# Performance work log

Measured on AMD Instinct MI355X. Metric: run time of the kernel, lower is better.

## Reference

```python
import jax, jax.numpy as jnp
import numpy as np

DIM = 512
HEADS = 6
DH = 64
INNER = HEADS * DH  # 384
M = 20              # num_landmarks
PINV_ITERS = 6
KERNEL = 33         # residual_conv_kernel
SCALE = DH ** -0.5


def setup_inputs() -> dict:
    key = jax.random.key(0)
    ks = jax.random.split(key, 7)
    x = jax.random.normal(ks[0], (16, 6000, DIM), dtype=jnp.float32)
    norm_w = jnp.ones((DIM,), dtype=jnp.float32)
    norm_b = jnp.zeros((DIM,), dtype=jnp.float32)
    w_qkv = jax.random.normal(ks[1], (DIM, 3 * INNER), dtype=jnp.float32) * 0.02
    w_out = jax.random.normal(ks[2], (INNER, DIM), dtype=jnp.float32) * 0.02
    b_out = jnp.zeros((DIM,), dtype=jnp.float32)
    # depthwise conv over seq dim: torch Conv2d(heads, heads, (33,1), groups=heads)
    res_kernel = jax.random.normal(ks[3], (HEADS, 1, KERNEL, 1), dtype=jnp.float32) * 0.1
    return {"x": x, "norm_w": norm_w, "norm_b": norm_b, "w_qkv": w_qkv,
            "w_out": w_out, "b_out": b_out, "res_kernel": res_kernel}


def moore_penrose_pinv(a, iters=PINV_ITERS):
    # a: [b, h, m, m]
    abs_a = jnp.abs(a)
    denom = abs_a.sum(-1).max() * abs_a.sum(-2).max()  # global maxes, as in torch ref
    z = jnp.swapaxes(a, -1, -2) / denom
    I = jnp.eye(a.shape[-1], dtype=a.dtype)
    for _ in range(iters):
        az = a @ z
        z = 0.25 * z @ (13.0 * I - az @ (15.0 * I - az @ (7.0 * I - az)))
    return z


def nystrom_attention(xn, w_qkv, w_out, b_out, res_kernel):
    b, n, _ = xn.shape
    qkv = xn @ w_qkv  # [b, n, 3*inner]
    q, k, v = jnp.split(qkv, 3, axis=-1)
    to_heads = lambda t: t.reshape(b, n, HEADS, DH).transpose(0, 2, 1, 3)  # b h n d
    q, k, v = to_heads(q), to_heads(k), to_heads(v)
    q = q * SCALE

    l = n // M  # n chosen as multiple of m, so no padding branch
    q_land = q.reshape(b, HEADS, M, l, DH).mean(axis=3)  # b h m d
    k_land = k.reshape(b, HEADS, M, l, DH).mean(axis=3)

    sim1 = jnp.einsum('bhid,bhjd->bhij', q, k_land)       # b h n m
    sim2 = jnp.einsum('bhid,bhjd->bhij', q_land, k_land)  # b h m m
    sim3 = jnp.einsum('bhid,bhjd->bhij', q_land, k)       # b h m n

    attn1 = jax.nn.softmax(sim1, axis=-1)
    attn2 = jax.nn.softmax(sim2, axis=-1)
    attn3 = jax.nn.softmax(sim3, axis=-1)

    attn2_inv = moore_penrose_pinv(attn2)
    out = (attn1 @ attn2_inv) @ (attn3 @ v)  # b h n d

    # residual depthwise conv along seq dim, per head (groups=heads)
    pad = KERNEL // 2
    conv = jax.lax.conv_general_dilated(
        v, res_kernel, window_strides=(1, 1), padding=((pad, pad), (0, 0)),
        dimension_numbers=('NCHW', 'OIHW', 'NCHW'), feature_group_count=HEADS)
    out = out + conv

    out = out.transpose(0, 2, 1, 3).reshape(b, n, INNER)
    return out @ w_out + b_out


def reference(x, norm_w, norm_b, w_qkv, w_out, b_out, res_kernel):
    mu = x.mean(-1, keepdims=True)
    var = jnp.mean((x - mu) ** 2, axis=-1, keepdims=True)
    xn = (x - mu) / jnp.sqrt(var + 1e-5) * norm_w + norm_b
    return x + nystrom_attention(xn, w_qkv, w_out, b_out, res_kernel)
```

## Files before the change

### kernel.cpp

```cpp
#include <hip/hip_runtime.h>

typedef float  f32x4  __attribute__((ext_vector_type(4)));
typedef __bf16 bf16x4 __attribute__((ext_vector_type(4)));
typedef __bf16 bf16x8 __attribute__((ext_vector_type(8)));

#define B_     16
#define N_     6000
#define D_     512
#define H_     6
#define DH_    64
#define INNER_ 384
#define M_     20
#define L_     300
#define KW_    33
#define ROWS_  (B_ * N_)
#define SCALE_ 0.125f
#define CH_    256
#define NCH_   24

__device__ __forceinline__ ushort f2bf(float f) {
    __bf16 h = (__bf16)f;
    return __builtin_bit_cast(ushort, h);
}
__device__ __forceinline__ float bf2f(ushort h) {
    return __uint_as_float(((unsigned)h) << 16);
}

#define GLD(gp, lp) __builtin_amdgcn_global_load_lds( \
    (const __attribute__((address_space(1))) unsigned int*)(gp), \
    (__attribute__((address_space(3))) unsigned int*)(lp), 16, 0, 0)

__global__ __launch_bounds__(256) void ln_kernel(const float* __restrict__ x,
        const float* __restrict__ w, const float* __restrict__ b,
        ushort* __restrict__ xn) {
    int row  = blockIdx.x * 4 + (threadIdx.x >> 6);
    int lane = threadIdx.x & 63;
    const float4* xp = (const float4*)(x + (size_t)row * D_);
    float4 v0 = xp[lane];
    float4 v1 = xp[lane + 64];
    float s  = v0.x + v0.y + v0.z + v0.w + v1.x + v1.y + v1.z + v1.w;
    float sq = v0.x*v0.x + v0.y*v0.y + v0.z*v0.z + v0.w*v0.w
             + v1.x*v1.x + v1.y*v1.y + v1.z*v1.z + v1.w*v1.w;
    #pragma unroll
    for (int o = 32; o; o >>= 1) { s += __shfl_xor(s, o); sq += __shfl_xor(sq, o); }
    float mu   = s * (1.0f / D_);
    float var  = sq * (1.0f / D_) - mu * mu;
    float rstd = rsqrtf(var + 1e-5f);
    const float4 wv0 = ((const float4*)w)[lane];
    const float4 wv1 = ((const float4*)w)[lane + 64];
    const float4 bv0 = ((const float4*)b)[lane];
    const float4 bv1 = ((const float4*)b)[lane + 64];
    ushort4 o0, o1;
    o0.x = f2bf((v0.x - mu) * rstd * wv0.x + bv0.x);
    o0.y = f2bf((v0.y - mu) * rstd * wv0.y + bv0.y);
    o0.z = f2bf((v0.z - mu) * rstd * wv0.z + bv0.z);
    o0.w = f2bf((v0.w - mu) * rstd * wv0.w + bv0.w);
    o1.x = f2bf((v1.x - mu) * rstd * wv1.x + bv1.x);
    o1.y = f2bf((v1.y - mu) * rstd * wv1.y + bv1.y);
    o1.z = f2bf((v1.z - mu) * rstd * wv1.z + bv1.z);
    o1.w = f2bf((v1.w - mu) * rstd * wv1.w + bv1.w);
    ((ushort4*)(xn + (size_t)row * D_))[lane]      = o0;
    ((ushort4*)(xn + (size_t)row * D_))[lane + 64] = o1;
}

__global__ void transpose_cast_kernel(const float* __restrict__ W, ushort* __restrict__ WT,
                                      int R, int C) {
    int idx = blockIdx.x * blockDim.x + threadIdx.x;
    if (idx >= R * C) return;
    int r = idx / C, c = idx - r * C;
    WT[(size_t)c * R + r] = f2bf(W[idx]);
}

template<int KDIM, int NT, int EPI>
__global__ __launch_bounds__(256) void gemm_kernel(
        const ushort* __restrict__ A, const ushort* __restrict__ BT,
        ushort* __restrict__ qo, ushort* __restrict__ ko, ushort* __restrict__ vo,
        float* __restrict__ outp, const float* __restrict__ xres, const float* __restrict__ bout) {
    __shared__ __align__(16) ushort As[128 * 32];
    __shared__ __align__(16) ushort Bs[128 * 32];

    const int nwg = (int)gridDim.x;
    const int orig = (int)blockIdx.x;
    const int qd = nwg >> 3, rm = nwg & 7;
    const int xcd = orig & 7, loc = orig >> 3;
    const int wg = (xcd < rm ? xcd * (qd + 1) : rm * (qd + 1) + (xcd - rm) * qd) + loc;
    const int m0 = (wg / NT) * 128, n0 = (wg % NT) * 128;

    const int tid = threadIdx.x;
    const int lane = tid & 63, wave = tid >> 6;
    const int wm = (wave >> 1) * 64, wn = (wave & 1) * 64;
    const int fr = lane & 15;

    const int seg0 = wave * 2, seg1 = wave * 2 + 1;
    const int srow0 = seg0 * 16 + (lane >> 2);
    const int srow1 = seg1 * 16 + (lane >> 2);
    const int scol  = ((((lane & 3) - ((lane >> 3) & 3)) & 3) * 8);
    const ushort* Ag0 = A  + (size_t)(m0 + srow0) * KDIM + scol;
    const ushort* Ag1 = A  + (size_t)(m0 + srow1) * KDIM + scol;
    const ushort* Bg0 = BT + (size_t)(n0 + srow0) * KDIM + scol;
    const ushort* Bg1 = BT + (size_t)(n0 + srow1) * KDIM + scol;
    ushort* Al0 = &As[seg0 * 512];
    ushort* Al1 = &As[seg1 * 512];
    ushort* Bl0 = &Bs[seg0 * 512];
    ushort* Bl1 = &Bs[seg1 * 512];

    const int rp = (((lane >> 4) + (fr >> 1)) & 3) * 8;

    f32x4 acc[4][4] = {};

    for (int k0 = 0; k0 < KDIM; k0 += 32) {
        __syncthreads();
        GLD(Ag0 + k0, Al0);
        GLD(Ag1 + k0, Al1);
        GLD(Bg0 + k0, Bl0);
        GLD(Bg1 + k0, Bl1);
        __syncthreads();
        bf16x8 af[4], bfv[4];
        #pragma unroll
        for (int i = 0; i < 4; ++i) {
            af[i]  = *(const bf16x8*)&As[(wm + i * 16 + fr) * 32 + rp];
            bfv[i] = *(const bf16x8*)&Bs[(wn + i * 16 + fr) * 32 + rp];
        }
        #pragma unroll
        for (int i = 0; i < 4; ++i)
            #pragma unroll
            for (int j = 0; j < 4; ++j)
                acc[i][j] = __builtin_amdgcn_mfma_f32_16x16x32_bf16(af[i], bfv[j], acc[i][j], 0, 0, 0);
    }

    #pragma unroll
    for (int i = 0; i < 4; ++i) {
        #pragma unroll
        for (int j = 0; j < 4; ++j) {
            #pragma unroll
            for (int rg = 0; rg < 4; ++rg) {
                int gr = m0 + wm + i * 16 + ((lane >> 4) << 2) + rg;
                int gc = n0 + wn + j * 16 + (lane & 15);
                float val = acc[i][j][rg];
                if (EPI == 0) {
                    int bb = gr / N_, ii = gr - bb * N_;
                    int part = gc / INNER_, rem = gc - part * INNER_;
                    int h = rem >> 6, d = rem & 63;
                    size_t di = (((size_t)bb * H_ + h) * N_ + ii) * DH_ + d;
                    if (part == 0)      qo[di] = f2bf(val * SCALE_);
                    else if (part == 1) ko[di] = f2bf(val);
                    else                vo[di] = f2bf(val);
                } else {
                    size_t oi = (size_t)gr * D_ + gc;
                    outp[oi] = val + bout[gc] + xres[oi];
                }
            }
        }
    }
}

__global__ __launch_bounds__(64) void landmark_kernel(const ushort* __restrict__ q,
        const ushort* __restrict__ k, float* __restrict__ qland, float* __restrict__ kland) {
    int bhm = blockIdx.x;
    int bh = bhm / M_, m = bhm - bh * M_;
    const ushort* src = (blockIdx.y == 0) ? q : k;
    float* dst = (blockIdx.y == 0) ? qland : kland;
    int d = threadIdx.x;
    const ushort* p = src + ((size_t)bh * N_ + m * L_) * DH_ + d;
    float s = 0.f;
    #pragma unroll 4
    for (int j = 0; j < L_; ++j) s += bf2f(p[(size_t)j * DH_]);
    dst[((size_t)bh * M_ + m) * DH_ + d] = s * (1.0f / L_);
}

__global__ __launch_bounds__(512) void attn2_kernel(const float* __restrict__ qland,
        const float* __restrict__ kland, float* __restrict__ attn2, unsigned* __restrict__ gmax) {
    int bh = blockIdx.x;
    __shared__ float sim[M_ * M_];
    int t = threadIdx.x;
    if (t < M_ * M_) {
        int i = t / M_, j = t - (t / M_) * M_;
        const float* qp = qland + ((size_t)bh * M_ + i) * DH_;
        const float* kp = kland + ((size_t)bh * M_ + j) * DH_;
        float s = 0.f;
        for (int d = 0; d < DH_; ++d) s += qp[d] * kp[d];
        sim[t] = s;
    }
    __syncthreads();
    if (t < M_) {
        float mx = -1e30f;
        for (int j = 0; j < M_; ++j) mx = fmaxf(mx, sim[t * M_ + j]);
        float s = 0.f;
        for (int j = 0; j < M_; ++j) { float e = __expf(sim[t * M_ + j] - mx); sim[t * M_ + j] = e; s += e; }
        float inv = 1.0f / s;
        for (int j = 0; j < M_; ++j) sim[t * M_ + j] *= inv;
    }
    __syncthreads();
    if (t < M_ * M_) attn2[(size_t)bh * 400 + t] = sim[t];
    if (t < M_) {
        float cs = 0.f, rs = 0.f;
        for (int i = 0; i < M_; ++i) { cs += sim[i * M_ + t]; rs += sim[t * M_ + i]; }
        atomicMax(&gmax[1], __float_as_uint(cs));
        atomicMax(&gmax[0], __float_as_uint(rs));
    }
}

__global__ __launch_bounds__(512) void pinv_kernel(const float* __restrict__ attn2,
        const unsigned* __restrict__ gmax, float* __restrict__ ainv) {
    int bh = blockIdx.x;
    __shared__ float buf[5 * 400];
    float* pa = buf; float* pz = buf + 400; float* m1 = buf + 800; float* m2 = buf + 1200; float* m3 = buf + 1600;
    int t = threadIdx.x;
    float rden = 1.0f / (__uint_as_float(gmax[0]) * __uint_as_float(gmax[1]));
    int i = t / M_, j = t - (t / M_) * M_;
    if (t < 400) {
        pa[t] = attn2[(size_t)bh * 400 + t];
        pz[t] = attn2[(size_t)bh * 400 + j * M_ + i] * rden;
    }
    for (int it = 0; it < 6; ++it) {
        __syncthreads();
        if (t < 400) { float s = 0; for (int kk = 0; kk < M_; ++kk) s += pa[i * M_ + kk] * pz[kk * M_ + j]; m1[t] = s; }
        __syncthreads();
        if (t < 400) { float s = 0; for (int kk = 0; kk < M_; ++kk) s += m1[i * M_ + kk] * m1[kk * M_ + j]; m2[t] = 7.0f * m1[t] - s; }
        __syncthreads();
        if (t < 400) { float s = 0; for (int kk = 0; kk < M_; ++kk) s += m1[i * M_ + kk] * m2[kk * M_ + j]; m3[t] = 15.0f * m1[t] - s; }
        __syncthreads();
        if (t < 400) { float s = 0; for (int kk = 0; kk < M_; ++kk) s += pz[i * M_ + kk] * m3[kk * M_ + j]; m2[t] = 0.25f * (13.0f * pz[t] - s); }
        __syncthreads();
        float* tmp = pz; pz = m2; m2 = tmp;
    }
    if (t < 400) ainv[(size_t)bh * 400 + t] = pz[t];
}

__global__ __launch_bounds__(256) void attn3v_partial_kernel(
        const float* __restrict__ qland, const ushort* __restrict__ k,
        const ushort* __restrict__ v, float* __restrict__ pacc, float* __restrict__ pden) {
    int ch = blockIdx.x, bh = blockIdx.y;
    __shared__ float  qld[M_ * DH_];
    __shared__ float  P[CH_][21];
    __shared__ ushort Vs[CH_ * DH_];
    int t = threadIdx.x;
    for (int i = t; i < M_ * DH_; i += 256) qld[i] = qland[(size_t)bh * M_ * DH_ + i];

    int j = ch * CH_ + t;
    bool valid = j < N_;
    int jc = valid ? j : N_ - 1;

    const uint4* vr = (const uint4*)(v + ((size_t)bh * N_ + jc) * DH_);
    #pragma unroll
    for (int c = 0; c < 8; ++c)
        *(uint4*)&Vs[t * 64 + ((c ^ (t & 7)) << 3)] = vr[c];

    float kf[64];
    const uint4* kr = (const uint4*)(k + ((size_t)bh * N_ + jc) * DH_);
    #pragma unroll
    for (int c = 0; c < 8; ++c) {
        uint4 u = kr[c];
        kf[c*8+0] = bf2f((ushort)(u.x & 0xFFFF)); kf[c*8+1] = bf2f((ushort)(u.x >> 16));
        kf[c*8+2] = bf2f((ushort)(u.y & 0xFFFF)); kf[c*8+3] = bf2f((ushort)(u.y >> 16));
        kf[c*8+4] = bf2f((ushort)(u.z & 0xFFFF)); kf[c*8+5] = bf2f((ushort)(u.z >> 16));
        kf[c*8+6] = bf2f((ushort)(u.w & 0xFFFF)); kf[c*8+7] = bf2f((ushort)(u.w >> 16));
    }
    __syncthreads();

    #pragma unroll 2
    for (int m = 0; m < M_; ++m) {
        const float4* q4 = (const float4*)&qld[m * DH_];
        float s = 0.f;
        #pragma unroll
        for (int d4 = 0; d4 < 16; ++d4) {
            float4 a = q4[d4];
            s += kf[d4*4+0]*a.x + kf[d4*4+1]*a.y + kf[d4*4+2]*a.z + kf[d4*4+3]*a.w;
        }
        P[t][m] = valid ? __expf(s) : 0.f;
    }
    __syncthreads();

    int d = t & 63, mb = t >> 6;
    int cch = d >> 3, drem = d & 7;
    float acc[5] = {0.f, 0.f, 0.f, 0.f, 0.f};
    for (int j2 = 0; j2 < CH_; j2 += 2) {
        float v0 = bf2f(Vs[j2 * 64 + ((cch ^ (j2 & 7)) << 3) + drem]);
        float v1 = bf2f(Vs[(j2+1) * 64 + ((cch ^ ((j2+1) & 7)) << 3) + drem]);
        #pragma unroll
        for (int r = 0; r < 5; ++r) {
            acc[r] += P[j2][mb + 4*r] * v0;
            acc[r] += P[j2+1][mb + 4*r] * v1;
        }
    }
    #pragma unroll
    for (int r = 0; r < 5; ++r)
        pacc[(((size_t)bh * NCH_ + ch) * M_ + (mb + 4*r)) * DH_ + d] = acc[r];

    if (t < M_) {
        float s = 0.f;
        for (int j2 = 0; j2 < CH_; ++j2) s += P[j2][t];
        pden[((size_t)bh * NCH_ + ch) * M_ + t] = s;
    }
}

__global__ __launch_bounds__(256) void akv_kernel(const float* __restrict__ ainv,
        const float* __restrict__ pacc, const float* __restrict__ pden,
        float* __restrict__ akv) {
    int bh = blockIdx.x;
    __shared__ float kvs[M_ * DH_];
    __shared__ float inv_s[M_ * M_];
    __shared__ float den[M_];
    int t = threadIdx.x;
    for (int i = t; i < M_ * M_; i += 256) inv_s[i] = ainv[(size_t)bh * 400 + i];
    if (t < M_) {
        float s = 0.f;
        for (int c = 0; c < NCH_; ++c) s += pden[((size_t)bh * NCH_ + c) * M_ + t];
        den[t] = s;
    }
    __syncthreads();
    for (int idx = t; idx < M_ * DH_; idx += 256) {
        int m = idx >> 6;
        float s = 0.f;
        #pragma unroll 4
        for (int c = 0; c < NCH_; ++c) s += pacc[((size_t)bh * NCH_ + c) * M_ * DH_ + idx];
        kvs[idx] = s / den[m];
    }
    __syncthreads();
    for (int idx = t; idx < M_ * DH_; idx += 256) {
        int m = idx >> 6, d = idx & 63;
        float s = 0.f;
        #pragma unroll
        for (int mm = 0; mm < M_; ++mm) s += inv_s[m * M_ + mm] * kvs[mm * DH_ + d];
        akv[(size_t)bh * M_ * DH_ + idx] = s;
    }
}

__global__ __launch_bounds__(256) void out_attn_kernel(const ushort* __restrict__ q,
        const ushort* __restrict__ v, const float* __restrict__ kland,
        const float* __restrict__ akv, const float* __restrict__ resk,
        ushort* __restrict__ att_out) {
    int bh = blockIdx.y;
    int b = bh / H_, h = bh - b * H_;
    int r0 = blockIdx.x * 64;
    __shared__ ushort Vs[96 * 64];
    __shared__ float  Cs[64 * 65];
    __shared__ float  klf[M_ * DH_];
    __shared__ float  akvs[M_ * DH_];
    int t = threadIdx.x;

    const ushort* vbase = v + (size_t)bh * N_ * DH_;
    #pragma unroll
    for (int i = 0; i < 3; ++i) {
        int c2 = t + i * 256;
        int row = c2 >> 3, ch = c2 & 7;
        int gr = r0 - 16 + row;
        uint4 val = make_uint4(0u, 0u, 0u, 0u);
        if (gr >= 0 && gr < N_) val = *(const uint4*)(vbase + (size_t)gr * DH_ + ch * 8);
        *(uint4*)&Vs[row * 64 + ch * 8] = val;
    }
    for (int i = t; i < M_ * DH_; i += 256) {
        klf[i]  = kland[(size_t)bh * M_ * DH_ + i];
        akvs[i] = akv[(size_t)bh * M_ * DH_ + i];
    }
    float kr[KW_];
    #pragma unroll
    for (int tt = 0; tt < KW_; ++tt) kr[tt] = resk[h * KW_ + tt];
    __syncthreads();

    {
        int g = t >> 6, d = t & 63;
        float vv[48];
        #pragma unroll
        for (int j = 0; j < 48; ++j) vv[j] = bf2f(Vs[(g * 16 + j) * 64 + d]);
        #pragma unroll
        for (int rr = 0; rr < 16; ++rr) {
            float s = 0.f;
            #pragma unroll
            for (int tt = 0; tt < KW_; ++tt) s += kr[tt] * vv[rr + tt];
            Cs[(g * 16 + rr) * 65 + d] = s;
        }
    }
    __syncthreads();

    int rr = t >> 2, quad = t & 3;
    int r = r0 + rr;
    bool valid = r < N_;
    int rc = valid ? r : N_ - 1;

    float qf[16];
    const uint4* qp = (const uint4*)(q + ((size_t)bh * N_ + rc) * DH_ + quad * 16);
    #pragma unroll
    for (int c = 0; c < 2; ++c) {
        uint4 u = qp[c];
        qf[c*8+0] = bf2f((ushort)(u.x & 0xFFFF)); qf[c*8+1] = bf2f((ushort)(u.x >> 16));
        qf[c*8+2] = bf2f((ushort)(u.y & 0xFFFF)); qf[c*8+3] = bf2f((ushort)(u.y >> 16));
        qf[c*8+4] = bf2f((ushort)(u.z & 0xFFFF)); qf[c*8+5] = bf2f((ushort)(u.z >> 16));
        qf[c*8+6] = bf2f((ushort)(u.w & 0xFFFF)); qf[c*8+7] = bf2f((ushort)(u.w >> 16));
    }

    float p[M_];
    #pragma unroll
    for (int m = 0; m < M_; ++m) {
        const float* kl = &klf[m * DH_ + quad * 16];
        float s = 0.f;
        #pragma unroll
        for (int dd = 0; dd < 16; ++dd) s += qf[dd] * kl[dd];
        s += __shfl_xor(s, 1);
        s += __shfl_xor(s, 2);
        p[m] = s;
    }
    float mx = -1e30f;
    #pragma unroll
    for (int m = 0; m < M_; ++m) mx = fmaxf(mx, p[m]);
    float ssum = 0.f;
    #pragma unroll
    for (int m = 0; m < M_; ++m) { p[m] = __expf(p[m] - mx); ssum += p[m]; }
    float rinv = 1.0f / ssum;
    #pragma unroll
    for (int m = 0; m < M_; ++m) p[m] *= rinv;

    float out[16];
    #pragma unroll
    for (int dd = 0; dd < 16; ++dd) out[dd] = Cs[rr * 65 + quad * 16 + dd];
    #pragma unroll
    for (int m = 0; m < M_; ++m) {
        float w = p[m];
        const float* av = &akvs[m * DH_ + quad * 16];
        #pragma unroll
        for (int dd = 0; dd < 16; ++dd) out[dd] += w * av[dd];
    }

    if (valid) {
        ushort* op = att_out + ((size_t)(b * N_ + r)) * INNER_ + h * DH_ + quad * 16;
        #pragma unroll
        for (int c = 0; c < 2; ++c) {
            uint4 w4;
            w4.x = (unsigned)f2bf(out[c*8+0]) | ((unsigned)f2bf(out[c*8+1]) << 16);
            w4.y = (unsigned)f2bf(out[c*8+2]) | ((unsigned)f2bf(out[c*8+3]) << 16);
            w4.z = (unsigned)f2bf(out[c*8+4]) | ((unsigned)f2bf(out[c*8+5]) << 16);
            w4.w = (unsigned)f2bf(out[c*8+6]) | ((unsigned)f2bf(out[c*8+7]) << 16);
            ((uint4*)op)[c] = w4;
        }
    }
}

extern "C" void kernel_launch(void* const* d_in, const int* in_sizes, int n_in,
                              void* d_out, int out_size, void* d_ws, size_t ws_size,
                              hipStream_t stream) {
    const float* x      = (const float*)d_in[0];
    const float* norm_w = (const float*)d_in[1];
    const float* norm_b = (const float*)d_in[2];
    const float* w_qkv  = (const float*)d_in[3];
    const float* w_out  = (const float*)d_in[4];
    const float* b_out  = (const float*)d_in[5];
    const float* res_k  = (const float*)d_in[6];

    char* wsp = (char*)d_ws;
    size_t off = 0;
    auto alloc = [&](size_t bytes) -> void* {
        void* p = wsp + off;
        off = (off + bytes + 255) & ~(size_t)255;
        return p;
    };
    ushort* xn    = (ushort*)alloc((size_t)ROWS_ * D_ * 2);
    ushort* qb    = (ushort*)alloc((size_t)B_ * H_ * N_ * DH_ * 2);
    ushort* kb    = (ushort*)alloc((size_t)B_ * H_ * N_ * DH_ * 2);
    ushort* vb    = (ushort*)alloc((size_t)B_ * H_ * N_ * DH_ * 2);
    ushort* wqkvT = (ushort*)alloc((size_t)3 * INNER_ * D_ * 2);
    ushort* woutT = (ushort*)alloc((size_t)D_ * INNER_ * 2);
    float*  qland = (float*)alloc((size_t)B_ * H_ * M_ * DH_ * 4);
    float*  kland = (float*)alloc((size_t)B_ * H_ * M_ * DH_ * 4);
    float*  attn2 = (float*)alloc((size_t)B_ * H_ * 400 * 4);
    float*  ainv  = (float*)alloc((size_t)B_ * H_ * 400 * 4);
    float*  pacc  = (float*)alloc((size_t)B_ * H_ * NCH_ * M_ * DH_ * 4);
    float*  pden  = (float*)alloc((size_t)B_ * H_ * NCH_ * M_ * 4);
    float*  akvb  = (float*)alloc((size_t)B_ * H_ * M_ * DH_ * 4);
    unsigned* gmx = (unsigned*)alloc(256);
    ushort* att_out = xn;

    hipMemsetAsync(gmx, 0, 8, stream);

    int tn = 3 * INNER_ * D_;
    transpose_cast_kernel<<<(tn + 255) / 256, 256, 0, stream>>>(w_qkv, wqkvT, D_, 3 * INNER_);
    tn = D_ * INNER_;
    transpose_cast_kernel<<<(tn + 255) / 256, 256, 0, stream>>>(w_out, woutT, INNER_, D_);

    ln_kernel<<<ROWS_ / 4, 256, 0, stream>>>(x, norm_w, norm_b, xn);

    gemm_kernel<D_, 9, 0><<<(ROWS_ / 128) * 9, 256, 0, stream>>>(
        xn, wqkvT, qb, kb, vb, nullptr, nullptr, nullptr);

    landmark_kernel<<<dim3(B_ * H_ * M_, 2), 64, 0, stream>>>(qb, kb, qland, kland);

    attn2_kernel<<<B_ * H_, 512, 0, stream>>>(qland, kland, attn2, gmx);
    pinv_kernel<<<B_ * H_, 512, 0, stream>>>(attn2, gmx, ainv);

    attn3v_partial_kernel<<<dim3(NCH_, B_ * H_), 256, 0, stream>>>(qland, kb, vb, pacc, pden);

    akv_kernel<<<B_ * H_, 256, 0, stream>>>(ainv, pacc, pden, akvb);

    out_attn_kernel<<<dim3((N_ + 63) / 64, B_ * H_), 256, 0, stream>>>(
        qb, vb, kland, akvb, res_k, att_out);

    gemm_kernel<INNER_, 4, 1><<<(ROWS_ / 128) * 4, 256, 0, stream>>>(
        att_out, woutT, nullptr, nullptr, nullptr, (float*)d_out, x, b_out);
}
```

Measured before the change: 669.5 us.

## Compute attn3·V partial sums with bf16 MFMA and smaller sequence chunks

Rewrites the landmark-by-key scores and the P·V accumulation in the attn3 partial kernel to use 16x16x32 bf16 MFMA instructions instead of scalar FP32 loops. K and V tiles are loaded straight into swizzled LDS with global_load_lds. The chunk size drops from 256 to 128 rows, which roughly doubles the number of blocks and the partial sums the akv reduction must add. The exp weights are now rounded to bf16 and the landmark queries are cast to bf16, so accuracy drops slightly.

```diff
diff --git a/kernel.cpp b/kernel.cpp
--- a/kernel.cpp
+++ b/kernel.cpp
@@ -15,8 +15,8 @@
 #define KW_    33
 #define ROWS_  (B_ * N_)
 #define SCALE_ 0.125f
-#define CH_    256
-#define NCH_   24
+#define CH2_   128
+#define NCH2_  47
 
 __device__ __forceinline__ ushort f2bf(float f) {
     __bf16 h = (__bf16)f;
@@ -227,70 +227,129 @@
     if (t < 400) ainv[(size_t)bh * 400 + t] = pz[t];
 }
 
-__global__ __launch_bounds__(256) void attn3v_partial_kernel(
+__global__ __launch_bounds__(256) void attn3v_mfma_kernel(
         const float* __restrict__ qland, const ushort* __restrict__ k,
         const ushort* __restrict__ v, float* __restrict__ pacc, float* __restrict__ pden) {
     int ch = blockIdx.x, bh = blockIdx.y;
-    __shared__ float  qld[M_ * DH_];
-    __shared__ float  P[CH_][21];
-    __shared__ ushort Vs[CH_ * DH_];
+    __shared__ __align__(16) ushort Ks[CH2_ * 64];
+    __shared__ __align__(16) ushort Vs[CH2_ * 64];
+    __shared__ __align__(16) ushort qlb[32 * 64];
+    __shared__ __align__(16) ushort Pt[32 * 136];
     int t = threadIdx.x;
-    for (int i = t; i < M_ * DH_; i += 256) qld[i] = qland[(size_t)bh * M_ * DH_ + i];
-
-    int j = ch * CH_ + t;
-    bool valid = j < N_;
-    int jc = valid ? j : N_ - 1;
-
-    const uint4* vr = (const uint4*)(v + ((size_t)bh * N_ + jc) * DH_);
-    #pragma unroll
-    for (int c = 0; c < 8; ++c)
-        *(uint4*)&Vs[t * 64 + ((c ^ (t & 7)) << 3)] = vr[c];
-
-    float kf[64];
-    const uint4* kr = (const uint4*)(k + ((size_t)bh * N_ + jc) * DH_);
-    #pragma unroll
-    for (int c = 0; c < 8; ++c) {
-        uint4 u = kr[c];
-        kf[c*8+0] = bf2f((ushort)(u.x & 0xFFFF)); kf[c*8+1] = bf2f((ushort)(u.x >> 16));
-        kf[c*8+2] = bf2f((ushort)(u.y & 0xFFFF)); kf[c*8+3] = bf2f((ushort)(u.y >> 16));
-        kf[c*8+4] = bf2f((ushort)(u.z & 0xFFFF)); kf[c*8+5] = bf2f((ushort)(u.z >> 16));
-        kf[c*8+6] = bf2f((ushort)(u.w & 0xFFFF)); kf[c*8+7] = bf2f((ushort)(u.w >> 16));
-    }
-    __syncthreads();
-
-    #pragma unroll 2
-    for (int m = 0; m < M_; ++m) {
-        const float4* q4 = (const float4*)&qld[m * DH_];
-        float s = 0.f;
-        #pragma unroll
-        for (int d4 = 0; d4 < 16; ++d4) {
-            float4 a = q4[d4];
-            s += kf[d4*4+0]*a.x + kf[d4*4+1]*a.y + kf[d4*4+2]*a.z + kf[d4*4+3]*a.w;
-        }
-        P[t][m] = valid ? __expf(s) : 0.f;
-    }
-    __syncthreads();
-
-    int d = t & 63, mb = t >> 6;
+    int lane = t & 63, wave = t >> 6;
+    int j0 = ch * CH2_;
+    int jmax = N_ - j0; if (jmax > CH2_) jmax = CH2_;
+
+    const ushort* kbase = k + ((size_t)bh * N_ + j0) * DH_;
+    const ushort* vbase = v + ((size_t)bh * N_ + j0) * DH_;
+    #pragma unroll
+    for (int i = 0; i < 4; ++i) {
+        int pdx = (wave * 4 + i) * 64 + lane;
+        int row = pdx >> 3, pp = pdx & 7;
+        int c = (pp - (row & 7)) & 7;
+        int rowc = row < jmax ? row : jmax - 1;
+        GLD(kbase + (size_t)rowc * DH_ + c * 8, &Ks[pdx * 8]);
+        GLD(vbase + (size_t)rowc * DH_ + c * 8, &Vs[pdx * 8]);
+    }
+    {
+        int row = t >> 3, pp = t & 7;
+        int c = (pp - (row & 7)) & 7;
+        ushort w8[8];
+        if (row < M_) {
+            const float* qp = qland + ((size_t)bh * M_ + row) * DH_ + c * 8;
+            #pragma unroll
+            for (int e = 0; e < 8; ++e) w8[e] = f2bf(qp[e]);
+        } else {
+            #pragma unroll
+            for (int e = 0; e < 8; ++e) w8[e] = 0;
+        }
+        *(uint4*)&qlb[t * 8] = *(const uint4*)w8;
+    }
+    __syncthreads();
+
+    int fr = lane & 15, g = lane >> 4;
+
+    f32x4 sacc[2][2] = {};
+    #pragma unroll
+    for (int ks = 0; ks < 2; ++ks) {
+        bf16x8 bq[2];
+        #pragma unroll
+        for (int mt = 0; mt < 2; ++mt) {
+            int m = mt * 16 + fr;
+            int c = ks * 4 + g;
+            int pp = (c + (m & 7)) & 7;
+            bq[mt] = *(const bf16x8*)&qlb[m * 64 + pp * 8];
+        }
+        #pragma unroll
+        for (int jl = 0; jl < 2; ++jl) {
+            int row = (wave * 2 + jl) * 16 + fr;
+            int c = ks * 4 + g;
+            int pp = (c + (row & 7)) & 7;
+            bf16x8 ak = *(const bf16x8*)&Ks[row * 64 + pp * 8];
+            #pragma unroll
+            for (int mt = 0; mt < 2; ++mt)
+                sacc[jl][mt] = __builtin_amdgcn_mfma_f32_16x16x32_bf16(ak, bq[mt], sacc[jl][mt], 0, 0, 0);
+        }
+    }
+    #pragma unroll
+    for (int jl = 0; jl < 2; ++jl) {
+        #pragma unroll
+        for (int mt = 0; mt < 2; ++mt) {
+            int m = mt * 16 + fr;
+            #pragma unroll
+            for (int rg = 0; rg < 4; ++rg) {
+                int jloc = (wave * 2 + jl) * 16 + 4 * g + rg;
+                float e = __expf(sacc[jl][mt][rg]);
+                e = (jloc < jmax) ? e : 0.f;
+                int c = jloc >> 3;
+                int pp = (c & 8) | ((c + (m & 7)) & 7);
+                Pt[m * 136 + pp * 8 + (jloc & 7)] = f2bf(e);
+            }
+        }
+    }
+    __syncthreads();
+
+    if (t < M_) {
+        float s = 0.f;
+        #pragma unroll
+        for (int cc = 0; cc < 16; ++cc) {
+            bf16x8 pv = *(const bf16x8*)&Pt[t * 136 + cc * 8];
+            #pragma unroll
+            for (int e = 0; e < 8; ++e) s += (float)pv[e];
+        }
+        pden[((size_t)bh * NCH2_ + ch) * M_ + t] = s;
+    }
+
+    f32x4 oacc[2] = {};
+    int d = wave * 16 + fr;
     int cch = d >> 3, drem = d & 7;
-    float acc[5] = {0.f, 0.f, 0.f, 0.f, 0.f};
-    for (int j2 = 0; j2 < CH_; j2 += 2) {
-        float v0 = bf2f(Vs[j2 * 64 + ((cch ^ (j2 & 7)) << 3) + drem]);
-        float v1 = bf2f(Vs[(j2+1) * 64 + ((cch ^ ((j2+1) & 7)) << 3) + drem]);
-        #pragma unroll
-        for (int r = 0; r < 5; ++r) {
-            acc[r] += P[j2][mb + 4*r] * v0;
-            acc[r] += P[j2+1][mb + 4*r] * v1;
-        }
-    }
-    #pragma unroll
-    for (int r = 0; r < 5; ++r)
-        pacc[(((size_t)bh * NCH_ + ch) * M_ + (mb + 4*r)) * DH_ + d] = acc[r];
-
-    if (t < M_) {
-        float s = 0.f;
-        for (int j2 = 0; j2 < CH_; ++j2) s += P[j2][t];
-        pden[((size_t)bh * NCH_ + ch) * M_ + t] = s;
+    #pragma unroll
+    for (int ks = 0; ks < 4; ++ks) {
+        ushort bw[8];
+        #pragma unroll
+        for (int e = 0; e < 8; ++e) {
+            int j = ks * 32 + g * 8 + e;
+            int pp = (cch + (j & 7)) & 7;
+            bw[e] = Vs[j * 64 + pp * 8 + drem];
+        }
+        bf16x8 bv = *(const bf16x8*)bw;
+        #pragma unroll
+        for (int mt = 0; mt < 2; ++mt) {
+            int m = mt * 16 + fr;
+            int c = ks * 4 + g;
+            int pp = (c & 8) | ((c + (m & 7)) & 7);
+            bf16x8 ap = *(const bf16x8*)&Pt[m * 136 + pp * 8];
+            oacc[mt] = __builtin_amdgcn_mfma_f32_16x16x32_bf16(ap, bv, oacc[mt], 0, 0, 0);
+        }
+    }
+    #pragma unroll
+    for (int mt = 0; mt < 2; ++mt) {
+        #pragma unroll
+        for (int rg = 0; rg < 4; ++rg) {
+            int m = mt * 16 + 4 * g + rg;
+            if (m < M_)
+                pacc[(((size_t)bh * NCH2_ + ch) * M_ + m) * DH_ + d] = oacc[mt][rg];
+        }
     }
 }
 
@@ -305,7 +364,7 @@
     for (int i = t; i < M_ * M_; i += 256) inv_s[i] = ainv[(size_t)bh * 400 + i];
     if (t < M_) {
         float s = 0.f;
-        for (int c = 0; c < NCH_; ++c) s += pden[((size_t)bh * NCH_ + c) * M_ + t];
+        for (int c = 0; c < NCH2_; ++c) s += pden[((size_t)bh * NCH2_ + c) * M_ + t];
         den[t] = s;
     }
     __syncthreads();
@@ -313,7 +372,7 @@
         int m = idx >> 6;
         float s = 0.f;
         #pragma unroll 4
-        for (int c = 0; c < NCH_; ++c) s += pacc[((size_t)bh * NCH_ + c) * M_ * DH_ + idx];
+        for (int c = 0; c < NCH2_; ++c) s += pacc[((size_t)bh * NCH2_ + c) * M_ * DH_ + idx];
         kvs[idx] = s / den[m];
     }
     __syncthreads();
@@ -463,8 +522,8 @@
     float*  kland = (float*)alloc((size_t)B_ * H_ * M_ * DH_ * 4);
     float*  attn2 = (float*)alloc((size_t)B_ * H_ * 400 * 4);
     float*  ainv  = (float*)alloc((size_t)B_ * H_ * 400 * 4);
-    float*  pacc  = (float*)alloc((size_t)B_ * H_ * NCH_ * M_ * DH_ * 4);
-    float*  pden  = (float*)alloc((size_t)B_ * H_ * NCH_ * M_ * 4);
+    float*  pacc  = (float*)alloc((size_t)B_ * H_ * NCH2_ * M_ * DH_ * 4);
+    float*  pden  = (float*)alloc((size_t)B_ * H_ * NCH2_ * M_ * 4);
     float*  akvb  = (float*)alloc((size_t)B_ * H_ * M_ * DH_ * 4);
     unsigned* gmx = (unsigned*)alloc(256);
     ushort* att_out = xn;
@@ -486,7 +545,7 @@
     attn2_kernel<<<B_ * H_, 512, 0, stream>>>(qland, kland, attn2, gmx);
     pinv_kernel<<<B_ * H_, 512, 0, stream>>>(attn2, gmx, ainv);
 
-    attn3v_partial_kernel<<<dim3(NCH_, B_ * H_), 256, 0, stream>>>(qland, kb, vb, pacc, pden);
+    attn3v_mfma_kernel<<<dim3(NCH2_, B_ * H_), 256, 0, stream>>>(qland, kb, vb, pacc, pden);
 
     akv_kernel<<<B_ * H_, 256, 0, stream>>>(ainv, pacc, pden, akvb);
 
```

New measurement: 610.6 us (median of 2 runs). 8.8% less time.
